# Optimization experiments

Measured on AMD Instinct MI355X. Metric: run time of the kernel, lower is better.

Reference implementation:

```python
import jax, jax.numpy as jnp
import numpy as np

N_ITER = 50  # entmax_bisect default iteration count


def _pclip(z, inv_am1):
    return jnp.clip(z, 0.0, None) ** inv_am1


def entmax_bisect(X, alpha, axis=1, n_iter=N_ITER):
    """alpha-entmax via bisection (entmax library algorithm). X: [B,L,1], alpha: [B,1,1]."""
    am1 = alpha - 1.0
    inv_am1 = 1.0 / am1
    Xs = X * am1
    max_val = jnp.max(Xs, axis=axis, keepdims=True)
    dsz = X.shape[axis]
    tau_lo = max_val - 1.0                      # gp(1, alpha) = 1
    tau_hi = max_val - (1.0 / dsz) ** am1       # gp(1/d, alpha)
    f_lo = jnp.sum(_pclip(Xs - tau_lo, inv_am1), axis=axis, keepdims=True) - 1.0
    dm0 = tau_hi - tau_lo
    p0 = _pclip(Xs - tau_lo, inv_am1)

    def body(_, carry):
        tau_lo, dm, _ = carry
        dm = dm * 0.5
        tau_m = tau_lo + dm
        p_m = _pclip(Xs - tau_m, inv_am1)
        f_m = jnp.sum(p_m, axis=axis, keepdims=True) - 1.0
        tau_lo = jnp.where(f_m * f_lo >= 0, tau_m, tau_lo)
        return tau_lo, dm, p_m

    _, _, p = jax.lax.fori_loop(0, n_iter, body, (tau_lo, dm0, p0))
    return p / jnp.sum(p, axis=axis, keepdims=True)  # ensure_sum_one


def setup_inputs() -> dict:
    key = jax.random.key(0)
    ks = jax.random.split(key, 11)
    n_items, d, B, L = 500000, 128, 1024, 200
    s = 1.0 / np.sqrt(d)
    return {
        "item_embedding": jax.random.normal(ks[0], (n_items, d), jnp.float32) * s,
        "items": jax.random.randint(ks[1], (B, L), 0, n_items, jnp.int64),
        "A": jax.random.uniform(ks[2], (B, B), jnp.float32) * (1.0 / B),
        "D": jax.random.uniform(ks[3], (B, B), jnp.float32) * (1.0 / B),
        "intention_embedding": jax.random.normal(ks[4], (B, 1, d), jnp.float32) * s,
        "atten_w0": jax.random.normal(ks[5], (1, d), jnp.float32) * s,
        "atten_w1": jax.random.normal(ks[6], (d, d), jnp.float32) * s,
        "atten_w2": jax.random.normal(ks[7], (d, d), jnp.float32) * s,
        "atten_bias": jax.random.normal(ks[8], (d,), jnp.float32) * s,
        "alpha_w_weight": jax.random.normal(ks[9], (1, d), jnp.float32) * s,
        "alpha_w_bias": jnp.zeros((1,), jnp.float32),
    }


def reference(item_embedding, items, A, D, intention_embedding,
              atten_w0, atten_w1, atten_w2, atten_bias,
              alpha_w_weight, alpha_w_bias):
    B, L = items.shape
    d = item_embedding.shape[1]
    seq_h = item_embedding[items]                      # [B, L, d] gather
    g = jnp.sum(seq_h, axis=1)                         # [B, d]
    DA = D @ A                                         # [B, B]
    g = DA @ g                                         # [B, d] GCN aggregation
    q = intention_embedding                            # [B, 1, d]
    # get_alpha: sigmoid(Linear(q)) + 1, with ==1 entries bumped to 1.00001
    alpha_ent = jax.nn.sigmoid(q @ alpha_w_weight.T + alpha_w_bias) + 1.0   # [B,1,1]
    alpha_ent = jnp.where(alpha_ent == 1.0, 1.00001, alpha_ent)
    k = jnp.broadcast_to(g[:, None, :], (B, L, d))     # k = v = expanded GCN emb
    h = jax.nn.relu(k @ atten_w1 + q @ atten_w2 + atten_bias)  # [B, L, d]
    scores = h @ atten_w0.T                            # [B, L, 1]
    p = entmax_bisect(scores, alpha_ent, axis=1)       # sparse attention over L
    c = jnp.einsum('blo,bld->bod', p, k)               # [B, 1, d]
    c = jax.nn.selu(c)[:, 0, :]                        # [B, d]
    return c / jnp.linalg.norm(c, axis=-1, keepdims=True)
```

## Files before the change

### kernel.cpp

```cpp
#include <hip/hip_runtime.h>
#include <math.h>

#define B_DIM 1024
#define L_DIM 200
#define D_DIM 128

__global__ __launch_bounds__(256) void k_gather(
    const float* __restrict__ emb,
    const int* __restrict__ items,
    float* __restrict__ g0,
    float* __restrict__ t,
    float* __restrict__ g) {
  const int b = blockIdx.x;
  const int tid = threadIdx.x;

  if (tid < D_DIM) {
    t[b * D_DIM + tid] = 0.f;
    g[b * D_DIM + tid] = 0.f;
  }

  __shared__ int sidx[L_DIM];
  if (tid < L_DIM) sidx[tid] = items[b * L_DIM + tid];
  __syncthreads();

  const int grp = tid >> 5;
  const int lane = tid & 31;

  float4 acc = make_float4(0.f, 0.f, 0.f, 0.f);
  for (int l = grp; l < L_DIM; l += 8) {
    const float4* p =
        reinterpret_cast<const float4*>(emb + (long long)sidx[l] * D_DIM) + lane;
    float4 v = *p;
    acc.x += v.x; acc.y += v.y; acc.z += v.z; acc.w += v.w;
  }

  __shared__ float4 red[8][32];
  red[grp][lane] = acc;
  __syncthreads();

  if (tid < D_DIM) {
    float s = 0.f;
#pragma unroll
    for (int j = 0; j < 8; ++j) {
      const float* rp = reinterpret_cast<const float*>(&red[j][0]);
      s += rp[tid];
    }
    g0[b * D_DIM + tid] = s;
  }
}

__global__ __launch_bounds__(256) void k_matmul_splitk(
    const float* __restrict__ A,
    const float* __restrict__ Bm,
    float* __restrict__ C) {
  const int rt = blockIdx.x;
  const int kc = blockIdx.y;
  const int tid = threadIdx.x;

  __shared__ float As[64][68];
  __shared__ float Bs[64][128];

#pragma unroll
  for (int i = 0; i < 4; ++i) {
    int tt = tid + i * 256;
    int r = tt >> 4;
    int k4 = (tt & 15) << 2;
    float4 v = *reinterpret_cast<const float4*>(
        A + (long long)(rt * 64 + r) * 1024 + kc * 64 + k4);
    *reinterpret_cast<float4*>(&As[r][k4]) = v;
  }
#pragma unroll
  for (int i = 0; i < 8; ++i) {
    int tt = tid + i * 256;
    int k = tt >> 5;
    int c4 = (tt & 31) << 2;
    float4 v = *reinterpret_cast<const float4*>(
        Bm + (long long)(kc * 64 + k) * 128 + c4);
    *reinterpret_cast<float4*>(&Bs[k][c4]) = v;
  }
  __syncthreads();

  const int tr = tid >> 5;
  const int tc = tid & 31;
  const int r0 = tr * 8;
  const int c0 = tc * 4;

  float acc[8][4];
#pragma unroll
  for (int i = 0; i < 8; ++i)
#pragma unroll
    for (int j = 0; j < 4; ++j) acc[i][j] = 0.f;

#pragma unroll 4
  for (int k = 0; k < 64; ++k) {
    float4 bv = *reinterpret_cast<const float4*>(&Bs[k][c0]);
#pragma unroll
    for (int i = 0; i < 8; ++i) {
      float a = As[r0 + i][k];
      acc[i][0] = fmaf(a, bv.x, acc[i][0]);
      acc[i][1] = fmaf(a, bv.y, acc[i][1]);
      acc[i][2] = fmaf(a, bv.z, acc[i][2]);
      acc[i][3] = fmaf(a, bv.w, acc[i][3]);
    }
  }

#pragma unroll
  for (int i = 0; i < 8; ++i) {
    int row = rt * 64 + r0 + i;
#pragma unroll
    for (int j = 0; j < 4; ++j) {
      atomicAdd(&C[row * 128 + c0 + j], acc[i][j]);
    }
  }
}

__global__ __launch_bounds__(128) void k_epilogue(const float* __restrict__ g,
                                                  float* __restrict__ out) {
  const int b = blockIdx.x;
  const int tid = threadIdx.x;
  const float sc = 1.0507009873554805f;
  const float al = 1.6732632423543772f;

  float v = g[b * D_DIM + tid];
  float y = v > 0.f ? sc * v : sc * al * expm1f(v);

  float ss = y * y;
#pragma unroll
  for (int o = 1; o < 64; o <<= 1) ss += __shfl_xor(ss, o, 64);

  __shared__ float wsum[2];
  if ((tid & 63) == 0) wsum[tid >> 6] = ss;
  __syncthreads();
  float tot = wsum[0] + wsum[1];

  out[b * D_DIM + tid] = y * (1.f / sqrtf(tot));
}

extern "C" void kernel_launch(void* const* d_in, const int* in_sizes, int n_in,
                              void* d_out, int out_size, void* d_ws,
                              size_t ws_size, hipStream_t stream) {
  const float* emb   = (const float*)d_in[0];
  const int*   items = (const int*)d_in[1];
  const float* A     = (const float*)d_in[2];
  const float* D     = (const float*)d_in[3];
  float* out = (float*)d_out;

  float* g0 = (float*)d_ws;
  float* t  = g0 + B_DIM * D_DIM;
  float* g  = t + B_DIM * D_DIM;

  k_gather<<<B_DIM, 256, 0, stream>>>(emb, items, g0, t, g);

  dim3 grid2(16, 16);
  k_matmul_splitk<<<grid2, 256, 0, stream>>>(A, g0, t);
  k_matmul_splitk<<<grid2, 256, 0, stream>>>(D, t, g);

  k_epilogue<<<B_DIM, 128, 0, stream>>>(g, out);
}
```

Measured before the change: 398.0 us.

## Replace split-K atomic accumulation with partial buffers and separate reduction kernels

Each split-K matmul block now writes its partial tile to a dedicated slice of a workspace buffer instead of atomically adding into the output. A reduce kernel sums the 16 partials for the intermediate product, and a fused reduce+SELU+normalize kernel does the same for the final one. The row tile shrinks from 64 to 32 rows to double the block count. This removes atomic contention and zero-init writes, at the cost of extra partial-buffer traffic and one additional kernel launch.

```diff
diff --git a/kernel.cpp b/kernel.cpp
--- a/kernel.cpp
+++ b/kernel.cpp
@@ -4,20 +4,17 @@
 #define B_DIM 1024
 #define L_DIM 200
 #define D_DIM 128
+#define KC_N 16
+#define KCHUNK 64
+#define RT_N 32
+#define RROWS 32
 
 __global__ __launch_bounds__(256) void k_gather(
     const float* __restrict__ emb,
     const int* __restrict__ items,
-    float* __restrict__ g0,
-    float* __restrict__ t,
-    float* __restrict__ g) {
+    float* __restrict__ g0) {
   const int b = blockIdx.x;
   const int tid = threadIdx.x;
-
-  if (tid < D_DIM) {
-    t[b * D_DIM + tid] = 0.f;
-    g[b * D_DIM + tid] = 0.f;
-  }
 
   __shared__ int sidx[L_DIM];
   if (tid < L_DIM) sidx[tid] = items[b * L_DIM + tid];
@@ -49,24 +46,24 @@
   }
 }
 
-__global__ __launch_bounds__(256) void k_matmul_splitk(
-    const float* __restrict__ A,
+__global__ __launch_bounds__(256) void k_mm_partial(
+    const float* __restrict__ M,
     const float* __restrict__ Bm,
-    float* __restrict__ C) {
+    float* __restrict__ P) {
   const int rt = blockIdx.x;
   const int kc = blockIdx.y;
   const int tid = threadIdx.x;
 
-  __shared__ float As[64][68];
-  __shared__ float Bs[64][128];
+  __shared__ float As[RROWS][KCHUNK + 4];
+  __shared__ float Bs[KCHUNK][D_DIM];
 
 #pragma unroll
-  for (int i = 0; i < 4; ++i) {
+  for (int i = 0; i < 2; ++i) {
     int tt = tid + i * 256;
     int r = tt >> 4;
     int k4 = (tt & 15) << 2;
     float4 v = *reinterpret_cast<const float4*>(
-        A + (long long)(rt * 64 + r) * 1024 + kc * 64 + k4);
+        M + (long long)(rt * RROWS + r) * B_DIM + kc * KCHUNK + k4);
     *reinterpret_cast<float4*>(&As[r][k4]) = v;
   }
 #pragma unroll
@@ -75,65 +72,82 @@
     int k = tt >> 5;
     int c4 = (tt & 31) << 2;
     float4 v = *reinterpret_cast<const float4*>(
-        Bm + (long long)(kc * 64 + k) * 128 + c4);
+        Bm + (long long)(kc * KCHUNK + k) * D_DIM + c4);
     *reinterpret_cast<float4*>(&Bs[k][c4]) = v;
   }
   __syncthreads();
 
-  const int tr = tid >> 5;
-  const int tc = tid & 31;
-  const int r0 = tr * 8;
-  const int c0 = tc * 4;
+  const int rr = tid >> 5;
+  const int cc = tid & 31;
+  const int r0 = rr * 4;
+  const int c0 = cc * 4;
 
-  float acc[8][4];
+  float acc[4][4];
 #pragma unroll
-  for (int i = 0; i < 8; ++i)
+  for (int i = 0; i < 4; ++i)
 #pragma unroll
     for (int j = 0; j < 4; ++j) acc[i][j] = 0.f;
 
 #pragma unroll 4
-  for (int k = 0; k < 64; ++k) {
+  for (int k = 0; k < KCHUNK; ++k) {
     float4 bv = *reinterpret_cast<const float4*>(&Bs[k][c0]);
-#pragma unroll
-    for (int i = 0; i < 8; ++i) {
-      float a = As[r0 + i][k];
-      acc[i][0] = fmaf(a, bv.x, acc[i][0]);
-      acc[i][1] = fmaf(a, bv.y, acc[i][1]);
-      acc[i][2] = fmaf(a, bv.z, acc[i][2]);
-      acc[i][3] = fmaf(a, bv.w, acc[i][3]);
-    }
+    float a0 = As[r0 + 0][k];
+    float a1 = As[r0 + 1][k];
+    float a2 = As[r0 + 2][k];
+    float a3 = As[r0 + 3][k];
+    acc[0][0] = fmaf(a0, bv.x, acc[0][0]); acc[0][1] = fmaf(a0, bv.y, acc[0][1]);
+    acc[0][2] = fmaf(a0, bv.z, acc[0][2]); acc[0][3] = fmaf(a0, bv.w, acc[0][3]);
+    acc[1][0] = fmaf(a1, bv.x, acc[1][0]); acc[1][1] = fmaf(a1, bv.y, acc[1][1]);
+    acc[1][2] = fmaf(a1, bv.z, acc[1][2]); acc[1][3] = fmaf(a1, bv.w, acc[1][3]);
+    acc[2][0] = fmaf(a2, bv.x, acc[2][0]); acc[2][1] = fmaf(a2, bv.y, acc[2][1]);
+    acc[2][2] = fmaf(a2, bv.z, acc[2][2]); acc[2][3] = fmaf(a2, bv.w, acc[2][3]);
+    acc[3][0] = fmaf(a3, bv.x, acc[3][0]); acc[3][1] = fmaf(a3, bv.y, acc[3][1]);
+    acc[3][2] = fmaf(a3, bv.z, acc[3][2]); acc[3][3] = fmaf(a3, bv.w, acc[3][3]);
   }
 
 #pragma unroll
-  for (int i = 0; i < 8; ++i) {
-    int row = rt * 64 + r0 + i;
-#pragma unroll
-    for (int j = 0; j < 4; ++j) {
-      atomicAdd(&C[row * 128 + c0 + j], acc[i][j]);
-    }
+  for (int i = 0; i < 4; ++i) {
+    int row = rt * RROWS + r0 + i;
+    *reinterpret_cast<float4*>(
+        &P[((long long)kc * B_DIM + row) * D_DIM + c0]) =
+        make_float4(acc[i][0], acc[i][1], acc[i][2], acc[i][3]);
   }
 }
 
-__global__ __launch_bounds__(128) void k_epilogue(const float* __restrict__ g,
-                                                  float* __restrict__ out) {
+__global__ __launch_bounds__(128) void k_reduce(const float* __restrict__ P,
+                                                float* __restrict__ T) {
   const int b = blockIdx.x;
-  const int tid = threadIdx.x;
+  const int c = threadIdx.x;
+  float s = 0.f;
+#pragma unroll
+  for (int kc = 0; kc < KC_N; ++kc)
+    s += P[((long long)kc * B_DIM + b) * D_DIM + c];
+  T[b * D_DIM + c] = s;
+}
+
+__global__ __launch_bounds__(128) void k_reduce_selu_norm(
+    const float* __restrict__ P, float* __restrict__ out) {
+  const int b = blockIdx.x;
+  const int c = threadIdx.x;
+  float s = 0.f;
+#pragma unroll
+  for (int kc = 0; kc < KC_N; ++kc)
+    s += P[((long long)kc * B_DIM + b) * D_DIM + c];
+
   const float sc = 1.0507009873554805f;
   const float al = 1.6732632423543772f;
-
-  float v = g[b * D_DIM + tid];
-  float y = v > 0.f ? sc * v : sc * al * expm1f(v);
+  float y = s > 0.f ? sc * s : sc * al * expm1f(s);
 
   float ss = y * y;
 #pragma unroll
   for (int o = 1; o < 64; o <<= 1) ss += __shfl_xor(ss, o, 64);
 
   __shared__ float wsum[2];
-  if ((tid & 63) == 0) wsum[tid >> 6] = ss;
+  if ((c & 63) == 0) wsum[c >> 6] = ss;
   __syncthreads();
   float tot = wsum[0] + wsum[1];
 
-  out[b * D_DIM + tid] = y * (1.f / sqrtf(tot));
+  out[b * D_DIM + c] = y * (1.f / sqrtf(tot));
 }
 
 extern "C" void kernel_launch(void* const* d_in, const int* in_sizes, int n_in,
@@ -146,14 +160,15 @@
   float* out = (float*)d_out;
 
   float* g0 = (float*)d_ws;
-  float* t  = g0 + B_DIM * D_DIM;
-  float* g  = t + B_DIM * D_DIM;
+  float* pA = g0 + B_DIM * D_DIM;
+  float* t  = pA + (long long)KC_N * B_DIM * D_DIM;
+  float* pB = t + B_DIM * D_DIM;
 
-  k_gather<<<B_DIM, 256, 0, stream>>>(emb, items, g0, t, g);
+  k_gather<<<B_DIM, 256, 0, stream>>>(emb, items, g0);
 
-  dim3 grid2(16, 16);
-  k_matmul_splitk<<<grid2, 256, 0, stream>>>(A, g0, t);
-  k_matmul_splitk<<<grid2, 256, 0, stream>>>(D, t, g);
-
-  k_epilogue<<<B_DIM, 128, 0, stream>>>(g, out);
+  dim3 gmm(RT_N, KC_N);
+  k_mm_partial<<<gmm, 256, 0, stream>>>(A, g0, pA);
+  k_reduce<<<B_DIM, 128, 0, stream>>>(pA, t);
+  k_mm_partial<<<gmm, 256, 0, stream>>>(D, t, pB);
+  k_reduce_selu_norm<<<B_DIM, 128, 0, stream>>>(pB, out);
 }
```

New measurement: 344.6 us. 1.16x faster.
